# Kernel optimization log

Measured on AMD Instinct MI355X. Metric: run time of the kernel, lower is better.

Reference implementation:

```python
import jax, jax.numpy as jnp
import numpy as np

D_MODEL, N_LAYERS, D_INNER, D_STATE, D_CONV, DT_RANK, NUM_CLASSES = 256, 4, 512, 16, 4, 16, 10
B, L = 8, 1024


def setup_inputs() -> dict:
    key = jax.random.key(0)
    ks = jax.random.split(key, 16)
    s = 0.02
    inp = {}
    inp['x'] = jax.random.normal(ks[0], (B, L, 1), jnp.float32)
    inp['input_w'] = jax.random.normal(ks[1], (D_MODEL, 1), jnp.float32) * s
    inp['input_b'] = jnp.zeros((D_MODEL,), jnp.float32)
    inp['ln_w'] = jnp.ones((N_LAYERS, D_MODEL), jnp.float32)
    inp['ln_b'] = jnp.zeros((N_LAYERS, D_MODEL), jnp.float32)
    inp['in_proj_w'] = jax.random.normal(ks[2], (N_LAYERS, 2 * D_INNER, D_MODEL), jnp.float32) * s
    inp['in_proj_b'] = jnp.zeros((N_LAYERS, 2 * D_INNER), jnp.float32)
    inp['conv_w'] = jax.random.normal(ks[3], (N_LAYERS, D_INNER, 1, D_CONV), jnp.float32) * 0.2
    inp['conv_b'] = jnp.zeros((N_LAYERS, D_INNER), jnp.float32)
    inp['x_proj_w'] = jax.random.normal(ks[4], (N_LAYERS, DT_RANK + 2 * D_STATE, D_INNER), jnp.float32) * s
    inp['dt_proj_w'] = jax.random.normal(ks[5], (N_LAYERS, D_INNER, DT_RANK), jnp.float32) * s
    inp['dt_proj_b'] = jax.random.normal(ks[6], (N_LAYERS, D_INNER), jnp.float32) * 0.1 - 4.0  # small softplus(dt)
    # canonical S4D-real init: A = [1..d_state] repeated over d_inner
    A = jnp.tile(jnp.arange(1, D_STATE + 1, dtype=jnp.float32)[None, :], (D_INNER, 1))
    inp['A_log'] = jnp.tile(jnp.log(A)[None], (N_LAYERS, 1, 1))
    inp['D'] = jnp.ones((N_LAYERS, D_INNER), jnp.float32)
    inp['out_proj_w'] = jax.random.normal(ks[7], (N_LAYERS, D_MODEL, D_INNER), jnp.float32) * s
    inp['out_proj_b'] = jnp.zeros((N_LAYERS, D_MODEL), jnp.float32)
    inp['norm_w'] = jnp.ones((D_MODEL,), jnp.float32)
    inp['norm_b'] = jnp.zeros((D_MODEL,), jnp.float32)
    inp['cls_w'] = jax.random.normal(ks[8], (NUM_CLASSES, D_MODEL), jnp.float32) * s
    inp['cls_b'] = jnp.zeros((NUM_CLASSES,), jnp.float32)
    return inp


def _layernorm(x, w, b, eps=1e-5):
    mu = jnp.mean(x, axis=-1, keepdims=True)
    var = jnp.mean(jnp.square(x - mu), axis=-1, keepdims=True)
    return (x - mu) * jax.lax.rsqrt(var + eps) * w + b


def _causal_depthwise_conv(u, w, b):
    # u: (B, L, D_inner), w: (D_inner, 1, K), causal padding K-1
    out = jax.lax.conv_general_dilated(
        u.transpose(0, 2, 1), w, window_strides=(1,), padding=[(D_CONV - 1, 0)],
        feature_group_count=D_INNER, dimension_numbers=('NCH', 'OIH', 'NCH'))
    return out.transpose(0, 2, 1) + b


def _selective_scan(u, delta, A, Bm, Cm, Dp):
    # u, delta: (B,L,Din); Bm, Cm: (B,L,N); A: (Din,N); Dp: (Din,)
    def step(h, inp):
        d_t, B_t, C_t, u_t = inp                       # (B,Din),(B,N),(B,N),(B,Din)
        dA = jnp.exp(d_t[:, :, None] * A)              # (B,Din,N)
        dBu = d_t[:, :, None] * B_t[:, None, :] * u_t[:, :, None]
        h = dA * h + dBu
        y = jnp.einsum('bdn,bn->bd', h, C_t)
        return h, y
    h0 = jnp.zeros((u.shape[0], D_INNER, D_STATE), u.dtype)
    xs = (delta.transpose(1, 0, 2), Bm.transpose(1, 0, 2), Cm.transpose(1, 0, 2), u.transpose(1, 0, 2))
    _, ys = jax.lax.scan(step, h0, xs)                 # ys: (L,B,Din)
    return ys.transpose(1, 0, 2) + u * Dp


def _mamba_layer(x, ln_w, ln_b, ipw, ipb, cw, cb, xpw, dtw, dtb, A_log, Dp, opw, opb):
    h = _layernorm(x, ln_w, ln_b)
    xz = jnp.einsum('bld,ed->ble', h, ipw) + ipb       # (B,L,2*Din)
    u, res = jnp.split(xz, 2, axis=-1)
    u = jax.nn.silu(_causal_depthwise_conv(u, cw, cb))
    x_dbl = jnp.einsum('bld,ed->ble', u, xpw)          # (B,L,dt_rank+2N)
    dt, Bm, Cm = jnp.split(x_dbl, [DT_RANK, DT_RANK + D_STATE], axis=-1)
    delta = jax.nn.softplus(jnp.einsum('blr,dr->bld', dt, dtw) + dtb)
    A = -jnp.exp(A_log)
    y = _selective_scan(u, delta, A, Bm, Cm, Dp)
    y = y * jax.nn.silu(res)
    return x + jnp.einsum('ble,de->bld', y, opw) + opb


def reference(x, input_w, input_b, ln_w, ln_b, in_proj_w, in_proj_b, conv_w, conv_b,
              x_proj_w, dt_proj_w, dt_proj_b, A_log, D, out_proj_w, out_proj_b,
              norm_w, norm_b, cls_w, cls_b):
    h = jnp.einsum('blc,dc->bld', x, input_w) + input_b   # (B,L,D_MODEL)
    for i in range(N_LAYERS):
        h = _mamba_layer(h, ln_w[i], ln_b[i], in_proj_w[i], in_proj_b[i], conv_w[i], conv_b[i],
                         x_proj_w[i], dt_proj_w[i], dt_proj_b[i], A_log[i], D[i],
                         out_proj_w[i], out_proj_b[i])
    h = _layernorm(h, norm_w, norm_b)
    pooled = jnp.mean(h, axis=1)                          # (B, D_MODEL)
    return jnp.einsum('bd,cd->bc', pooled, cls_w) + cls_b
```

## Files before the change

### kernel.cpp

```cpp
#include <hip/hip_runtime.h>
#include <hip/hip_bf16.h>
#include <math.h>

#define DM 256
#define NL 4
#define DI 512
#define DS 16
#define DC 4
#define DR 16
#define NC 10
#define NB 8
#define LL 1024
#define MR (NB*LL)
#define NCHUNK 64
#define CLEN 16

typedef __attribute__((ext_vector_type(4))) float f32x4;
typedef __attribute__((ext_vector_type(8))) short short8;

extern "C" __device__ float __ocml_native_exp2_f32(float);
__device__ __forceinline__ float exp2_f(float x) { return __ocml_native_exp2_f32(x); }
#define L2E 1.442695040888963f

__device__ __forceinline__ float silu_f(float x) {
    return x * (1.0f / (1.0f + __expf(-x)));
}
__device__ __forceinline__ float bf2f(ushort v) {
    union { unsigned u; float f; } c; c.u = ((unsigned)v) << 16; return c.f;
}
__device__ __forceinline__ ushort f2bf(float f) {
    union { float f; unsigned u; } c; c.f = f;
    unsigned lsb = (c.u >> 16) & 1;
    return (ushort)((c.u + 0x7fffu + lsb) >> 16);
}
__device__ __forceinline__ void g2lds16(const void* g, void* l) {
    __builtin_amdgcn_global_load_lds((const __attribute__((address_space(1))) void*)g,
                                     (__attribute__((address_space(3))) void*)l, 16, 0, 0);
}

#define IPW_N (NL*2*DI*DM)
#define XPW_N (NL*64*DI)
#define OPW_N (NL*DM*DI)
__global__ __launch_bounds__(256) void convert_weights_kernel(
        const float* __restrict__ ipw, const float* __restrict__ xpw,
        const float* __restrict__ opw,
        ushort* __restrict__ ipw_b, ushort* __restrict__ xpw_b, ushort* __restrict__ opw_b) {
    int t = blockIdx.x * 256 + threadIdx.x;
    if (t < IPW_N) { ipw_b[t] = f2bf(ipw[t]); return; }
    t -= IPW_N;
    if (t < XPW_N) {
        int l = t >> 15, r = (t >> 9) & 63, k = t & 511;
        xpw_b[t] = (r < 48) ? f2bf(xpw[((size_t)l * 48 + r) * DI + k]) : (ushort)0;
        return;
    }
    t -= XPW_N;
    if (t < OPW_N) opw_b[t] = f2bf(opw[t]);
}

__global__ __launch_bounds__(256) void input_ln_kernel(
        const float* __restrict__ x, const float* __restrict__ iw,
        const float* __restrict__ ib,
        const float* __restrict__ lnw, const float* __restrict__ lnb,
        float* __restrict__ hres, ushort* __restrict__ hln) {
    int row = blockIdx.x, t = threadIdx.x;
    float v = x[row] * iw[t] + ib[t];
    float s = v, q = v * v;
#pragma unroll
    for (int o = 32; o >= 1; o >>= 1) { s += __shfl_xor(s, o); q += __shfl_xor(q, o); }
    __shared__ float red[8];
    int wid = t >> 6;
    if ((t & 63) == 0) { red[wid] = s; red[4 + wid] = q; }
    __syncthreads();
    s = red[0] + red[1] + red[2] + red[3];
    q = red[4] + red[5] + red[6] + red[7];
    float mu = s * (1.0f / DM);
    float var = q * (1.0f / DM) - mu * mu;
    float rs = rsqrtf(var + 1e-5f);
    hres[row * DM + t] = v;
    hln[row * DM + t] = f2bf((v - mu) * rs * lnw[t] + lnb[t]);
}

template<int BM, int BN, int WM, int WN, int MODE>
__global__ __launch_bounds__(256) void mfma_gemm_kernel(
        const ushort* __restrict__ A, int lda,
        const ushort* __restrict__ W,
        const float* __restrict__ bias,
        ushort* __restrict__ Cb, float* __restrict__ Cf, int ldc, int K) {
    constexpr int FM = BM / WM / 16;
    constexpr int FN = BN / WN / 16;
    __shared__ __align__(16) char smem[(BM + BN) * 128];
    const int tid = threadIdx.x;
    const int l = tid & 63, w = tid >> 6;
    const int wr = w / WN, wc = w % WN;
    const int bm = blockIdx.x * BM, bn = blockIdx.y * BN;
    const int ldw = K;

    f32x4 acc[FM][FN] = {};

    for (int k0 = 0; k0 < K; k0 += 64) {
#pragma unroll
        for (int i = 0; i < (BM * 128 / 16) / 256; i++) {
            int lin = (i * 256 + tid) * 16;
            int q = lin ^ (((lin >> 7) & 7) << 4);
            g2lds16(A + (size_t)(bm + (q >> 7)) * lda + k0 + ((q & 127) >> 1), smem + lin);
        }
#pragma unroll
        for (int i = 0; i < (BN * 128 / 16) / 256; i++) {
            int lin = (i * 256 + tid) * 16;
            int q = lin ^ (((lin >> 7) & 7) << 4);
            g2lds16(W + (size_t)(bn + (q >> 7)) * ldw + k0 + ((q & 127) >> 1),
                    smem + BM * 128 + lin);
        }
        __syncthreads();
        const int rl = l & 15;
        const int kb0 = ((l >> 4) << 3) * 2;
#pragma unroll
        for (int kk = 0; kk < 2; kk++) {
            short8 af[FM], bfr[FN];
#pragma unroll
            for (int m = 0; m < FM; m++) {
                int off = (wr * (BM / WM) + m * 16 + rl) * 128 + kk * 64 + kb0;
                off ^= ((off >> 7) & 7) << 4;
                af[m] = *(const short8*)(smem + off);
            }
#pragma unroll
            for (int n = 0; n < FN; n++) {
                int off = (wc * (BN / WN) + n * 16 + rl) * 128 + kk * 64 + kb0;
                off ^= ((off >> 7) & 7) << 4;
                bfr[n] = *(const short8*)(smem + BM * 128 + off);
            }
#pragma unroll
            for (int m = 0; m < FM; m++)
#pragma unroll
                for (int n = 0; n < FN; n++)
                    acc[m][n] = __builtin_amdgcn_mfma_f32_16x16x32_bf16(
                        af[m], bfr[n], acc[m][n], 0, 0, 0);
        }
        __syncthreads();
    }

    const int row0 = bm + wr * (BM / WM) + ((l >> 4) << 2);
    const int col0 = bn + wc * (BN / WN) + (l & 15);
#pragma unroll
    for (int m = 0; m < FM; m++) {
#pragma unroll
        for (int n = 0; n < FN; n++) {
            int col = col0 + n * 16;
            float bv = (MODE == 1) ? 0.f : bias[col];
#pragma unroll
            for (int r = 0; r < 4; r++) {
                size_t idx = (size_t)(row0 + m * 16 + r) * ldc + col;
                float v = acc[m][n][r];
                if (MODE == 0) Cb[idx] = f2bf(v + bv);
                else Cf[idx] = v;
            }
        }
    }
}

__global__ __launch_bounds__(256) void outproj_ln_kernel(
        const ushort* __restrict__ A,
        const ushort* __restrict__ W,
        const float* __restrict__ bias,
        float* __restrict__ hres,
        const float* __restrict__ lnw, const float* __restrict__ lnb,
        ushort* __restrict__ hln) {
    constexpr int K = DI;
    __shared__ __align__(16) char smem[(32 + 256) * 128];
    const int tid = threadIdx.x;
    const int l = tid & 63, w = tid >> 6;
    const int bm = blockIdx.x * 32;

    f32x4 acc[2][4] = {};

    for (int k0 = 0; k0 < K; k0 += 64) {
        {
            int lin = tid * 16;
            int q = lin ^ (((lin >> 7) & 7) << 4);
            g2lds16(A + (size_t)(bm + (q >> 7)) * K + k0 + ((q & 127) >> 1), smem + lin);
        }
#pragma unroll
        for (int i = 0; i < 8; i++) {
            int lin = (i * 256 + tid) * 16;
            int q = lin ^ (((lin >> 7) & 7) << 4);
            g2lds16(W + (size_t)(q >> 7) * K + k0 + ((q & 127) >> 1), smem + 32 * 128 + lin);
        }
        __syncthreads();
        const int rl = l & 15;
        const int kb0 = ((l >> 4) << 3) * 2;
#pragma unroll
        for (int kk = 0; kk < 2; kk++) {
            short8 af[2], bfr[4];
#pragma unroll
            for (int m = 0; m < 2; m++) {
                int off = (m * 16 + rl) * 128 + kk * 64 + kb0;
                off ^= ((off >> 7) & 7) << 4;
                af[m] = *(const short8*)(smem + off);
            }
#pragma unroll
            for (int n = 0; n < 4; n++) {
                int off = (w * 64 + n * 16 + rl) * 128 + kk * 64 + kb0;
                off ^= ((off >> 7) & 7) << 4;
                bfr[n] = *(const short8*)(smem + 32 * 128 + off);
            }
#pragma unroll
            for (int m = 0; m < 2; m++)
#pragma unroll
                for (int n = 0; n < 4; n++)
                    acc[m][n] = __builtin_amdgcn_mfma_f32_16x16x32_bf16(
                        af[m], bfr[n], acc[m][n], 0, 0, 0);
        }
        __syncthreads();
    }

    const int r0 = (l >> 4) << 2;
    const int col0 = w * 64 + (l & 15);
    float vv[2][4][4];
    float s[2][4], q[2][4];
#pragma unroll
    for (int m = 0; m < 2; m++)
#pragma unroll
        for (int r = 0; r < 4; r++) { s[m][r] = 0.f; q[m][r] = 0.f; }
#pragma unroll
    for (int m = 0; m < 2; m++) {
#pragma unroll
        for (int n = 0; n < 4; n++) {
            int col = col0 + n * 16;
            float bv = bias[col];
#pragma unroll
            for (int r = 0; r < 4; r++) {
                int row = bm + r0 + m * 16 + r;
                float x = acc[m][n][r] + bv + hres[(size_t)row * DM + col];
                vv[m][n][r] = x;
                s[m][r] += x;
                q[m][r] += x * x;
            }
        }
    }
#pragma unroll
    for (int o = 1; o < 16; o <<= 1) {
#pragma unroll
        for (int m = 0; m < 2; m++)
#pragma unroll
            for (int r = 0; r < 4; r++) {
                s[m][r] += __shfl_xor(s[m][r], o);
                q[m][r] += __shfl_xor(q[m][r], o);
            }
    }
    float* red  = (float*)smem;
    float* redq = red + 128;
    if ((l & 15) == 0) {
#pragma unroll
        for (int m = 0; m < 2; m++)
#pragma unroll
            for (int r = 0; r < 4; r++) {
                int rl2 = r0 + m * 16 + r;
                red[rl2 * 4 + w] = s[m][r];
                redq[rl2 * 4 + w] = q[m][r];
            }
    }
    __syncthreads();
#pragma unroll
    for (int m = 0; m < 2; m++) {
        float mu[4], rs[4];
#pragma unroll
        for (int r = 0; r < 4; r++) {
            int rl2 = r0 + m * 16 + r;
            float ts = red[rl2 * 4] + red[rl2 * 4 + 1] + red[rl2 * 4 + 2] + red[rl2 * 4 + 3];
            float tq = redq[rl2 * 4] + redq[rl2 * 4 + 1] + redq[rl2 * 4 + 2] + redq[rl2 * 4 + 3];
            mu[r] = ts * (1.0f / DM);
            float var = tq * (1.0f / DM) - mu[r] * mu[r];
            rs[r] = rsqrtf(var + 1e-5f);
        }
#pragma unroll
        for (int n = 0; n < 4; n++) {
            int col = col0 + n * 16;
            float lw = lnw[col], lb = lnb[col];
#pragma unroll
            for (int r = 0; r < 4; r++) {
                int row = bm + r0 + m * 16 + r;
                hres[(size_t)row * DM + col] = vv[m][n][r];
                hln[(size_t)row * DM + col] = f2bf((vv[m][n][r] - mu[r]) * rs[r] * lw + lb);
            }
        }
    }
}

__global__ __launch_bounds__(256) void conv_silu_kernel(const ushort* __restrict__ xz,
        const float* __restrict__ cw, const float* __restrict__ cb, ushort* __restrict__ u) {
    int t = blockIdx.x * 256 + threadIdx.x;
    int d8 = (t & 63) << 3;
    int m = t >> 6;
    int l = m & (LL - 1);
    const short8 zr = {0, 0, 0, 0, 0, 0, 0, 0};
    const size_t base = (size_t)m * 1024 + d8;
    short8 r3 = *(const short8*)(xz + base);
    short8 r2 = (l >= 1) ? *(const short8*)(xz + base - 1024) : zr;
    short8 r1 = (l >= 2) ? *(const short8*)(xz + base - 2048) : zr;
    short8 r0 = (l >= 3) ? *(const short8*)(xz + base - 3072) : zr;
    short8 o;
#pragma unroll
    for (int j = 0; j < 8; j++) {
        int d = d8 + j;
        float4 w4 = *reinterpret_cast<const float4*>(&cw[d * 4]);
        float a = cb[d] + w4.w * bf2f((ushort)r3[j]);
        a += w4.z * bf2f((ushort)r2[j]);
        a += w4.y * bf2f((ushort)r1[j]);
        a += w4.x * bf2f((ushort)r0[j]);
        o[j] = (short)f2bf(silu_f(a));
    }
    *(short8*)(u + (size_t)m * DI + d8) = o;
}

__global__ __launch_bounds__(256, 4) void scan_phase1_kernel(
        const ushort* __restrict__ u, const float* __restrict__ x_dbl,
        const float* __restrict__ A_log,
        const float* __restrict__ dtw, const float* __restrict__ dtb,
        const float* __restrict__ Dp,
        float* __restrict__ sdv, float* __restrict__ Sbuf,
        unsigned* __restrict__ cy) {
    __shared__ __align__(16) float xs[CLEN * 64];
    const int tid = threadIdx.x;
    const int bc = blockIdx.x >> 1;
    const int d = ((blockIdx.x & 1) << 8) + tid;
    const int c = bc & (NCHUNK - 1);
    const int b = bc >> 6;
    const int m0 = b * LL + c * CLEN;
    *reinterpret_cast<float4*>(&xs[tid * 4]) =
        *reinterpret_cast<const float4*>(&x_dbl[(size_t)m0 * 64 + tid * 4]);

    float Aval[DS], h[DS], wreg[DR];
#pragma unroll
    for (int q = 0; q < 4; q++) {
        float4 a4 = *reinterpret_cast<const float4*>(&A_log[d * DS + q * 4]);
        Aval[q*4+0] = -__expf(a4.x) * L2E; Aval[q*4+1] = -__expf(a4.y) * L2E;
        Aval[q*4+2] = -__expf(a4.z) * L2E; Aval[q*4+3] = -__expf(a4.w) * L2E;
        float4 w4 = *reinterpret_cast<const float4*>(&dtw[d * DR + q * 4]);
        wreg[q*4] = w4.x; wreg[q*4+1] = w4.y; wreg[q*4+2] = w4.z; wreg[q*4+3] = w4.w;
    }
    float dbv = dtb[d];
    float Dval = Dp[d];
#pragma unroll
    for (int n = 0; n < DS; n++) h[n] = 0.f;
    const ushort* up = u + (size_t)m0 * DI + d;
    unsigned* cyp = cy + (size_t)m0 * DI + d;
    float sd = 0.f;
    __syncthreads();
    float uv = bf2f(up[0]);
    for (int t = 0; t < CLEN; t++) {
        float uvn = (t + 1 < CLEN) ? bf2f(up[(size_t)(t + 1) * DI]) : 0.f;
        const float* xr = &xs[t * 64];
        float4 x0 = *reinterpret_cast<const float4*>(xr);
        float4 x1 = *reinterpret_cast<const float4*>(xr + 4);
        float4 x2 = *reinterpret_cast<const float4*>(xr + 8);
        float4 x3 = *reinterpret_cast<const float4*>(xr + 12);
        float4 B0 = *reinterpret_cast<const float4*>(xr + 16);
        float4 B1 = *reinterpret_cast<const float4*>(xr + 20);
        float4 B2 = *reinterpret_cast<const float4*>(xr + 24);
        float4 B3 = *reinterpret_cast<const float4*>(xr + 28);
        float4 C0 = *reinterpret_cast<const float4*>(xr + 32);
        float4 C1 = *reinterpret_cast<const float4*>(xr + 36);
        float4 C2 = *reinterpret_cast<const float4*>(xr + 40);
        float4 C3 = *reinterpret_cast<const float4*>(xr + 44);
        float p0 = dbv + wreg[0]*x0.x + wreg[1]*x0.y + wreg[2]*x0.z + wreg[3]*x0.w;
        float p1 = wreg[4]*x1.x + wreg[5]*x1.y + wreg[6]*x1.z + wreg[7]*x1.w;
        float p2 = wreg[8]*x2.x + wreg[9]*x2.y + wreg[10]*x2.z + wreg[11]*x2.w;
        float p3 = wreg[12]*x3.x + wreg[13]*x3.y + wreg[14]*x3.z + wreg[15]*x3.w;
        float z = (p0 + p1) + (p2 + p3);
        float dv = (z > 20.0f) ? z : __logf(1.0f + __expf(z));
        sd += dv;
        float du = dv * uv;
        float a0, a1, a2, a3;
        h[0]  = exp2_f(dv*Aval[0])  * h[0]  + du * B0.x;  a0  = h[0]  * C0.x;
        h[1]  = exp2_f(dv*Aval[1])  * h[1]  + du * B0.y;  a0 += h[1]  * C0.y;
        h[2]  = exp2_f(dv*Aval[2])  * h[2]  + du * B0.z;  a0 += h[2]  * C0.z;
        h[3]  = exp2_f(dv*Aval[3])  * h[3]  + du * B0.w;  a0 += h[3]  * C0.w;
        h[4]  = exp2_f(dv*Aval[4])  * h[4]  + du * B1.x;  a1  = h[4]  * C1.x;
        h[5]  = exp2_f(dv*Aval[5])  * h[5]  + du * B1.y;  a1 += h[5]  * C1.y;
        h[6]  = exp2_f(dv*Aval[6])  * h[6]  + du * B1.z;  a1 += h[6]  * C1.z;
        h[7]  = exp2_f(dv*Aval[7])  * h[7]  + du * B1.w;  a1 += h[7]  * C1.w;
        h[8]  = exp2_f(dv*Aval[8])  * h[8]  + du * B2.x;  a2  = h[8]  * C2.x;
        h[9]  = exp2_f(dv*Aval[9])  * h[9]  + du * B2.y;  a2 += h[9]  * C2.y;
        h[10] = exp2_f(dv*Aval[10]) * h[10] + du * B2.z;  a2 += h[10] * C2.z;
        h[11] = exp2_f(dv*Aval[11]) * h[11] + du * B2.w;  a2 += h[11] * C2.w;
        h[12] = exp2_f(dv*Aval[12]) * h[12] + du * B3.x;  a3  = h[12] * C3.x;
        h[13] = exp2_f(dv*Aval[13]) * h[13] + du * B3.y;  a3 += h[13] * C3.y;
        h[14] = exp2_f(dv*Aval[14]) * h[14] + du * B3.z;  a3 += h[14] * C3.z;
        h[15] = exp2_f(dv*Aval[15]) * h[15] + du * B3.w;  a3 += h[15] * C3.w;
        float yv = ((a0 + a1) + (a2 + a3)) + Dval * uv;
        cyp[(size_t)t * DI] = (unsigned)f2bf(sd) | ((unsigned)f2bf(yv) << 16);
        uv = uvn;
    }
    size_t base = ((size_t)((b * NCHUNK + c) * DI + d)) * DS;
#pragma unroll
    for (int q = 0; q < 4; q++)
        *reinterpret_cast<float4*>(&Sbuf[base + q * 4]) =
            make_float4(h[q*4], h[q*4+1], h[q*4+2], h[q*4+3]);
    sdv[(b * NCHUNK + c) * DI + d] = sd;
}

__global__ __launch_bounds__(256) void scan_phase2_kernel(
        const float* __restrict__ sdv, const float* __restrict__ A_log,
        float* __restrict__ Sbuf) {
    int gid = blockIdx.x * 256 + threadIdx.x;
    int dn = gid & (DI * DS - 1);
    int b = gid >> 13;
    int n = dn & 15, d = dn >> 4;
    float Aval = -__expf(A_log[d * DS + n]) * L2E;
    size_t idx0 = (size_t)b * NCHUNK * DI * DS + dn;
    const size_t stride = (size_t)DI * DS;
    int sb0 = b * NCHUNK * DI + d;
    float h = 0.f;
    float S0[8], sd0[8];
#pragma unroll
    for (int j = 0; j < 8; j++) {
        S0[j] = Sbuf[idx0 + (size_t)j * stride];
        sd0[j] = sdv[sb0 + j * DI];
    }
    for (int g = 0; g < 8; g++) {
        float S1[8], sd1[8];
        if (g < 7) {
            int c1 = g * 8 + 8;
#pragma unroll
            for (int j = 0; j < 8; j++) {
                S1[j] = Sbuf[idx0 + (size_t)(c1 + j) * stride];
                sd1[j] = sdv[sb0 + (c1 + j) * DI];
            }
        } else {
#pragma unroll
            for (int j = 0; j < 8; j++) { S1[j] = 0.f; sd1[j] = 0.f; }
        }
#pragma unroll
        for (int j = 0; j < 8; j++) {
            float P = exp2_f(Aval * sd0[j]);
            Sbuf[idx0 + (size_t)(g * 8 + j) * stride] = h;
            h = P * h + S0[j];
        }
#pragma unroll
        for (int j = 0; j < 8; j++) { S0[j] = S1[j]; sd0[j] = sd1[j]; }
    }
}

__global__ __launch_bounds__(256, 4) void scan_phase3_kernel(
        const unsigned* __restrict__ cy,
        const float* __restrict__ x_dbl, const float* __restrict__ A_log,
        const float* __restrict__ Sbuf,
        const ushort* __restrict__ xz, ushort* __restrict__ y) {
    __shared__ __align__(16) float cs[CLEN * 16];
    const int tid = threadIdx.x;
    const int bc = blockIdx.x >> 1;
    const int d = ((blockIdx.x & 1) << 8) + tid;
    const int c = bc & (NCHUNK - 1);
    const int b = bc >> 6;
    const int m0 = b * LL + c * CLEN;
    {
        int tt = tid >> 4, k = tid & 15;
        cs[tt * 16 + k] = x_dbl[(size_t)(m0 + tt) * 64 + 32 + k];
    }
    float Aval[DS], hi[DS];
#pragma unroll
    for (int q = 0; q < 4; q++) {
        float4 a4 = *reinterpret_cast<const float4*>(&A_log[d * DS + q * 4]);
        Aval[q*4+0] = -__expf(a4.x) * L2E; Aval[q*4+1] = -__expf(a4.y) * L2E;
        Aval[q*4+2] = -__expf(a4.z) * L2E; Aval[q*4+3] = -__expf(a4.w) * L2E;
    }
    size_t base = ((size_t)((b * NCHUNK + c) * DI + d)) * DS;
#pragma unroll
    for (int q = 0; q < 4; q++) {
        float4 h4 = *reinterpret_cast<const float4*>(&Sbuf[base + q * 4]);
        hi[q*4] = h4.x; hi[q*4+1] = h4.y; hi[q*4+2] = h4.z; hi[q*4+3] = h4.w;
    }
    const unsigned* cyp = cy + (size_t)m0 * DI + d;
    const ushort* rp = xz + (size_t)m0 * 1024 + 512 + d;
    ushort* yp = y + (size_t)m0 * DI + d;
    __syncthreads();
    unsigned cyw = cyp[0];
    float rv = bf2f(rp[0]);
#pragma unroll 4
    for (int t = 0; t < CLEN; t++) {
        unsigned cywn = 0; float rvn = 0.f;
        if (t + 1 < CLEN) {
            cywn = cyp[(size_t)(t + 1) * DI];
            rvn = bf2f(rp[(size_t)(t + 1) * 1024]);
        }
        float cd = bf2f((ushort)(cyw & 0xffffu));
        float yl = bf2f((ushort)(cyw >> 16));
        const float* cr = &cs[t * 16];
        float4 C0 = *reinterpret_cast<const float4*>(cr);
        float4 C1 = *reinterpret_cast<const float4*>(cr + 4);
        float4 C2 = *reinterpret_cast<const float4*>(cr + 8);
        float4 C3 = *reinterpret_cast<const float4*>(cr + 12);
        float a0, a1, a2, a3;
        a0  = exp2_f(Aval[0]  * cd) * hi[0]  * C0.x;
        a0 += exp2_f(Aval[1]  * cd) * hi[1]  * C0.y;
        a0 += exp2_f(Aval[2]  * cd) * hi[2]  * C0.z;
        a0 += exp2_f(Aval[3]  * cd) * hi[3]  * C0.w;
        a1  = exp2_f(Aval[4]  * cd) * hi[4]  * C1.x;
        a1 += exp2_f(Aval[5]  * cd) * hi[5]  * C1.y;
        a1 += exp2_f(Aval[6]  * cd) * hi[6]  * C1.z;
        a1 += exp2_f(Aval[7]  * cd) * hi[7]  * C1.w;
        a2  = exp2_f(Aval[8]  * cd) * hi[8]  * C2.x;
        a2 += exp2_f(Aval[9]  * cd) * hi[9]  * C2.y;
        a2 += exp2_f(Aval[10] * cd) * hi[10] * C2.z;
        a2 += exp2_f(Aval[11] * cd) * hi[11] * C2.w;
        a3  = exp2_f(Aval[12] * cd) * hi[12] * C3.x;
        a3 += exp2_f(Aval[13] * cd) * hi[13] * C3.y;
        a3 += exp2_f(Aval[14] * cd) * hi[14] * C3.z;
        a3 += exp2_f(Aval[15] * cd) * hi[15] * C3.w;
        float yv = yl + ((a0 + a1) + (a2 + a3));
        yp[(size_t)t * DI] = f2bf(yv * silu_f(rv));
        cyw = cywn; rv = rvn;
    }
}

__global__ __launch_bounds__(256) void pool_partial_kernel(const ushort* __restrict__ ln,
                                                           float* __restrict__ partial) {
    int bs = blockIdx.x;
    int b = bs >> 3, sl = bs & 7;
    int t = threadIdx.x;
    int l0 = sl * 128;
    float s = 0.f;
    for (int l = 0; l < 128; l++) s += bf2f(ln[(size_t)(b * LL + l0 + l) * DM + t]);
    partial[(bs << 8) + t] = s;
}

__global__ void cls_kernel(const float* __restrict__ partial, const float* __restrict__ cw,
                           const float* __restrict__ cb, float* __restrict__ out) {
    int t = threadIdx.x;
    if (t >= NB * NC) return;
    int b = t / NC, c = t % NC;
    float s = 0.f;
    for (int k = 0; k < DM; k++) {
        float p = 0.f;
#pragma unroll
        for (int sl = 0; sl < 8; sl++) p += partial[((b * 8 + sl) << 8) + k];
        s += p * cw[c * DM + k];
    }
    out[t] = cb[c] + s * (1.0f / LL);
}

extern "C" void kernel_launch(void* const* d_in, const int* in_sizes, int n_in,
                              void* d_out, int out_size, void* d_ws, size_t ws_size,
                              hipStream_t stream) {
    const float* x       = (const float*)d_in[0];
    const float* input_w = (const float*)d_in[1];
    const float* input_b = (const float*)d_in[2];
    const float* ln_w    = (const float*)d_in[3];
    const float* ln_b    = (const float*)d_in[4];
    const float* ipw     = (const float*)d_in[5];
    const float* ipb     = (const float*)d_in[6];
    const float* cw      = (const float*)d_in[7];
    const float* cb      = (const float*)d_in[8];
    const float* xpw     = (const float*)d_in[9];
    const float* dtw     = (const float*)d_in[10];
    const float* dtb     = (const float*)d_in[11];
    const float* A_log   = (const float*)d_in[12];
    const float* Dp      = (const float*)d_in[13];
    const float* opw     = (const float*)d_in[14];
    const float* opb     = (const float*)d_in[15];
    const float* norm_w  = (const float*)d_in[16];
    const float* norm_b  = (const float*)d_in[17];
    const float* cls_w   = (const float*)d_in[18];
    const float* cls_b   = (const float*)d_in[19];
    float* out = (float*)d_out;
    float* ws = (float*)d_ws;

    float*    hres   = ws;
    ushort*   xz     = (ushort*)(hres + (size_t)MR * DM);
    ushort*   ub     = xz + (size_t)MR * 1024;
    float*    x_dbl  = (float*)(ub + (size_t)MR * DI);
    float*    sdvb   = x_dbl + (size_t)MR * 64;
    float*    Sbuf   = sdvb + (size_t)NB * NCHUNK * DI;
    float*    partial= Sbuf + (size_t)NB * NCHUNK * DI * DS;
    ushort*   ygate  = (ushort*)(partial + 64 * 256);
    ushort*   hln    = ygate + (size_t)MR * DI;
    ushort*   ipw_b  = hln + (size_t)MR * DM;
    ushort*   xpw_b  = ipw_b + IPW_N;
    ushort*   opw_b  = xpw_b + XPW_N;
    unsigned* cy     = (unsigned*)(opw_b + OPW_N);

    convert_weights_kernel<<<(IPW_N + XPW_N + OPW_N) / 256, 256, 0, stream>>>(
        ipw, xpw, opw, ipw_b, xpw_b, opw_b);
    input_ln_kernel<<<MR, 256, 0, stream>>>(x, input_w, input_b, ln_w, ln_b, hres, hln);

    for (int i = 0; i < NL; i++) {
        mfma_gemm_kernel<128, 128, 2, 2, 0><<<dim3(MR / 128, 1024 / 128), 256, 0, stream>>>(
            hln, DM, ipw_b + (size_t)i * 2 * DI * DM, ipb + (size_t)i * 2 * DI,
            xz, nullptr, 1024, DM);
        conv_silu_kernel<<<MR * DI / 8 / 256, 256, 0, stream>>>(xz, cw + i * DI * DC, cb + i * DI, ub);
        mfma_gemm_kernel<64, 64, 4, 1, 1><<<dim3(MR / 64, 1), 256, 0, stream>>>(
            ub, DI, xpw_b + (size_t)i * 64 * DI, nullptr, nullptr, x_dbl, 64, DI);
        scan_phase1_kernel<<<NB * NCHUNK * 2, 256, 0, stream>>>(
            ub, x_dbl, A_log + i * DI * DS, dtw + i * DI * DR, dtb + i * DI,
            Dp + i * DI, sdvb, Sbuf, cy);
        scan_phase2_kernel<<<NB * DI * DS / 256, 256, 0, stream>>>(
            sdvb, A_log + i * DI * DS, Sbuf);
        scan_phase3_kernel<<<NB * NCHUNK * 2, 256, 0, stream>>>(
            cy, x_dbl, A_log + i * DI * DS, Sbuf, xz, ygate);
        const float* nlw = (i < NL - 1) ? (ln_w + (i + 1) * DM) : norm_w;
        const float* nlb = (i < NL - 1) ? (ln_b + (i + 1) * DM) : norm_b;
        outproj_ln_kernel<<<MR / 32, 256, 0, stream>>>(
            ygate, opw_b + (size_t)i * DM * DI, opb + (size_t)i * DM,
            hres, nlw, nlb, hln);
    }

    pool_partial_kernel<<<64, 256, 0, stream>>>(hln, partial);
    cls_kernel<<<1, 128, 0, stream>>>(partial, cls_w, cls_b, out);
}
```

Measured before the change: 426.6 us.

## Halve scan chunk length to double chunk parallelism and precompute A values

The chunked selective scan now uses 128 chunks of 8 timesteps instead of 64 chunks of 16, doubling the number of blocks in phases 1 and 3 so more of the GPU is occupied. The cost is a longer sequential combine in phase 2 and twice as much chunk-state traffic through Sbuf. The -exp(A_log)*log2e values are computed once in the weight-conversion kernel and stored in a buffer, so the scan kernels no longer recompute them. The inner time loops are also fully unrolled.

```diff
diff --git a/kernel.cpp b/kernel.cpp
--- a/kernel.cpp
+++ b/kernel.cpp
@@ -12,8 +12,8 @@
 #define NB 8
 #define LL 1024
 #define MR (NB*LL)
-#define NCHUNK 64
-#define CLEN 16
+#define NCHUNK 128
+#define CLEN 8
 
 typedef __attribute__((ext_vector_type(4))) float f32x4;
 typedef __attribute__((ext_vector_type(8))) short short8;
@@ -41,10 +41,12 @@
 #define IPW_N (NL*2*DI*DM)
 #define XPW_N (NL*64*DI)
 #define OPW_N (NL*DM*DI)
+#define AV_N  (NL*DI*DS)
 __global__ __launch_bounds__(256) void convert_weights_kernel(
         const float* __restrict__ ipw, const float* __restrict__ xpw,
-        const float* __restrict__ opw,
-        ushort* __restrict__ ipw_b, ushort* __restrict__ xpw_b, ushort* __restrict__ opw_b) {
+        const float* __restrict__ opw, const float* __restrict__ A_log,
+        ushort* __restrict__ ipw_b, ushort* __restrict__ xpw_b,
+        ushort* __restrict__ opw_b, float* __restrict__ Av) {
     int t = blockIdx.x * 256 + threadIdx.x;
     if (t < IPW_N) { ipw_b[t] = f2bf(ipw[t]); return; }
     t -= IPW_N;
@@ -54,7 +56,9 @@
         return;
     }
     t -= XPW_N;
-    if (t < OPW_N) opw_b[t] = f2bf(opw[t]);
+    if (t < OPW_N) { opw_b[t] = f2bf(opw[t]); return; }
+    t -= OPW_N;
+    if (t < AV_N) Av[t] = -__expf(A_log[t]) * L2E;
 }
 
 __global__ __launch_bounds__(256) void input_ln_kernel(
@@ -314,7 +318,7 @@
 
 __global__ __launch_bounds__(256, 4) void scan_phase1_kernel(
         const ushort* __restrict__ u, const float* __restrict__ x_dbl,
-        const float* __restrict__ A_log,
+        const float* __restrict__ Av,
         const float* __restrict__ dtw, const float* __restrict__ dtb,
         const float* __restrict__ Dp,
         float* __restrict__ sdv, float* __restrict__ Sbuf,
@@ -324,17 +328,16 @@
     const int bc = blockIdx.x >> 1;
     const int d = ((blockIdx.x & 1) << 8) + tid;
     const int c = bc & (NCHUNK - 1);
-    const int b = bc >> 6;
+    const int b = bc >> 7;
     const int m0 = b * LL + c * CLEN;
-    *reinterpret_cast<float4*>(&xs[tid * 4]) =
-        *reinterpret_cast<const float4*>(&x_dbl[(size_t)m0 * 64 + tid * 4]);
+    *reinterpret_cast<float2*>(&xs[tid * 2]) =
+        *reinterpret_cast<const float2*>(&x_dbl[(size_t)m0 * 64 + tid * 2]);
 
     float Aval[DS], h[DS], wreg[DR];
 #pragma unroll
     for (int q = 0; q < 4; q++) {
-        float4 a4 = *reinterpret_cast<const float4*>(&A_log[d * DS + q * 4]);
-        Aval[q*4+0] = -__expf(a4.x) * L2E; Aval[q*4+1] = -__expf(a4.y) * L2E;
-        Aval[q*4+2] = -__expf(a4.z) * L2E; Aval[q*4+3] = -__expf(a4.w) * L2E;
+        float4 a4 = *reinterpret_cast<const float4*>(&Av[d * DS + q * 4]);
+        Aval[q*4+0] = a4.x; Aval[q*4+1] = a4.y; Aval[q*4+2] = a4.z; Aval[q*4+3] = a4.w;
         float4 w4 = *reinterpret_cast<const float4*>(&dtw[d * DR + q * 4]);
         wreg[q*4] = w4.x; wreg[q*4+1] = w4.y; wreg[q*4+2] = w4.z; wreg[q*4+3] = w4.w;
     }
@@ -347,6 +350,7 @@
     float sd = 0.f;
     __syncthreads();
     float uv = bf2f(up[0]);
+#pragma unroll
     for (int t = 0; t < CLEN; t++) {
         float uvn = (t + 1 < CLEN) ? bf2f(up[(size_t)(t + 1) * DI]) : 0.f;
         const float* xr = &xs[t * 64];
@@ -400,13 +404,13 @@
 }
 
 __global__ __launch_bounds__(256) void scan_phase2_kernel(
-        const float* __restrict__ sdv, const float* __restrict__ A_log,
+        const float* __restrict__ sdv, const float* __restrict__ Av,
         float* __restrict__ Sbuf) {
     int gid = blockIdx.x * 256 + threadIdx.x;
     int dn = gid & (DI * DS - 1);
     int b = gid >> 13;
     int n = dn & 15, d = dn >> 4;
-    float Aval = -__expf(A_log[d * DS + n]) * L2E;
+    float Aval = Av[d * DS + n];
     size_t idx0 = (size_t)b * NCHUNK * DI * DS + dn;
     const size_t stride = (size_t)DI * DS;
     int sb0 = b * NCHUNK * DI + d;
@@ -417,9 +421,9 @@
         S0[j] = Sbuf[idx0 + (size_t)j * stride];
         sd0[j] = sdv[sb0 + j * DI];
     }
-    for (int g = 0; g < 8; g++) {
+    for (int g = 0; g < NCHUNK / 8; g++) {
         float S1[8], sd1[8];
-        if (g < 7) {
+        if (g < NCHUNK / 8 - 1) {
             int c1 = g * 8 + 8;
 #pragma unroll
             for (int j = 0; j < 8; j++) {
@@ -443,7 +447,7 @@
 
 __global__ __launch_bounds__(256, 4) void scan_phase3_kernel(
         const unsigned* __restrict__ cy,
-        const float* __restrict__ x_dbl, const float* __restrict__ A_log,
+        const float* __restrict__ x_dbl, const float* __restrict__ Av,
         const float* __restrict__ Sbuf,
         const ushort* __restrict__ xz, ushort* __restrict__ y) {
     __shared__ __align__(16) float cs[CLEN * 16];
@@ -451,22 +455,18 @@
     const int bc = blockIdx.x >> 1;
     const int d = ((blockIdx.x & 1) << 8) + tid;
     const int c = bc & (NCHUNK - 1);
-    const int b = bc >> 6;
+    const int b = bc >> 7;
     const int m0 = b * LL + c * CLEN;
-    {
+    if (tid < CLEN * 16) {
         int tt = tid >> 4, k = tid & 15;
-        cs[tt * 16 + k] = x_dbl[(size_t)(m0 + tt) * 64 + 32 + k];
+        cs[tid] = x_dbl[(size_t)(m0 + tt) * 64 + 32 + k];
     }
     float Aval[DS], hi[DS];
+    size_t base = ((size_t)((b * NCHUNK + c) * DI + d)) * DS;
 #pragma unroll
     for (int q = 0; q < 4; q++) {
-        float4 a4 = *reinterpret_cast<const float4*>(&A_log[d * DS + q * 4]);
-        Aval[q*4+0] = -__expf(a4.x) * L2E; Aval[q*4+1] = -__expf(a4.y) * L2E;
-        Aval[q*4+2] = -__expf(a4.z) * L2E; Aval[q*4+3] = -__expf(a4.w) * L2E;
-    }
-    size_t base = ((size_t)((b * NCHUNK + c) * DI + d)) * DS;
-#pragma unroll
-    for (int q = 0; q < 4; q++) {
+        float4 a4 = *reinterpret_cast<const float4*>(&Av[d * DS + q * 4]);
+        Aval[q*4+0] = a4.x; Aval[q*4+1] = a4.y; Aval[q*4+2] = a4.z; Aval[q*4+3] = a4.w;
         float4 h4 = *reinterpret_cast<const float4*>(&Sbuf[base + q * 4]);
         hi[q*4] = h4.x; hi[q*4+1] = h4.y; hi[q*4+2] = h4.z; hi[q*4+3] = h4.w;
     }
@@ -476,7 +476,7 @@
     __syncthreads();
     unsigned cyw = cyp[0];
     float rv = bf2f(rp[0]);
-#pragma unroll 4
+#pragma unroll
     for (int t = 0; t < CLEN; t++) {
         unsigned cywn = 0; float rvn = 0.f;
         if (t + 1 < CLEN) {
@@ -577,10 +577,11 @@
     ushort*   ipw_b  = hln + (size_t)MR * DM;
     ushort*   xpw_b  = ipw_b + IPW_N;
     ushort*   opw_b  = xpw_b + XPW_N;
-    unsigned* cy     = (unsigned*)(opw_b + OPW_N);
-
-    convert_weights_kernel<<<(IPW_N + XPW_N + OPW_N) / 256, 256, 0, stream>>>(
-        ipw, xpw, opw, ipw_b, xpw_b, opw_b);
+    float*    Avbuf  = (float*)(opw_b + OPW_N);
+    unsigned* cy     = (unsigned*)(Avbuf + AV_N);
+
+    convert_weights_kernel<<<(IPW_N + XPW_N + OPW_N + AV_N) / 256, 256, 0, stream>>>(
+        ipw, xpw, opw, A_log, ipw_b, xpw_b, opw_b, Avbuf);
     input_ln_kernel<<<MR, 256, 0, stream>>>(x, input_w, input_b, ln_w, ln_b, hres, hln);
 
     for (int i = 0; i < NL; i++) {
@@ -591,12 +592,12 @@
         mfma_gemm_kernel<64, 64, 4, 1, 1><<<dim3(MR / 64, 1), 256, 0, stream>>>(
             ub, DI, xpw_b + (size_t)i * 64 * DI, nullptr, nullptr, x_dbl, 64, DI);
         scan_phase1_kernel<<<NB * NCHUNK * 2, 256, 0, stream>>>(
-            ub, x_dbl, A_log + i * DI * DS, dtw + i * DI * DR, dtb + i * DI,
+            ub, x_dbl, Avbuf + (size_t)i * DI * DS, dtw + i * DI * DR, dtb + i * DI,
             Dp + i * DI, sdvb, Sbuf, cy);
         scan_phase2_kernel<<<NB * DI * DS / 256, 256, 0, stream>>>(
-            sdvb, A_log + i * DI * DS, Sbuf);
+            sdvb, Avbuf + (size_t)i * DI * DS, Sbuf);
         scan_phase3_kernel<<<NB * NCHUNK * 2, 256, 0, stream>>>(
-            cy, x_dbl, A_log + i * DI * DS, Sbuf, xz, ygate);
+            cy, x_dbl, Avbuf + (size_t)i * DI * DS, Sbuf, xz, ygate);
         const float* nlw = (i < NL - 1) ? (ln_w + (i + 1) * DM) : norm_w;
         const float* nlb = (i < NL - 1) ? (ln_b + (i + 1) * DM) : norm_b;
         outproj_ln_kernel<<<MR / 32, 256, 0, stream>>>(
```

After: 437.5 us. 2.6% more time.
